# Performance work log

Hardware: AMD Instinct MI355X
Metric: run time of the kernel (lower is better)

The kernel has to match this reference:

```python
import jax, jax.numpy as jnp
import numpy as np

NUM_NODES = 100000
NUM_EDGES = 625000
IN_FEATURES = 128
OUT_FEATURES = 128


def setup_inputs() -> dict:
    key = jax.random.key(0)
    k1, k2, k3, k4 = jax.random.split(key, 4)
    x = jax.random.normal(k1, (NUM_NODES, IN_FEATURES), dtype=jnp.float32)
    edge_index = jax.random.randint(k2, (2, NUM_EDGES), 0, NUM_NODES, dtype=jnp.int64)
    # Xavier uniform for W (fan_in=IN, fan_out=OUT); B initialized to zeros in the
    # original, but we use small random values so gradients flow through both paths.
    limit = float(np.sqrt(6.0 / (IN_FEATURES + OUT_FEATURES)))
    W = jax.random.uniform(k3, (OUT_FEATURES, IN_FEATURES), dtype=jnp.float32,
                           minval=-limit, maxval=limit)
    B = jax.random.uniform(k4, (OUT_FEATURES, IN_FEATURES), dtype=jnp.float32,
                           minval=-limit, maxval=limit)
    return {"x": x, "edge_index": edge_index, "W": W, "B": B}


def reference(x, edge_index, W, B):
    sources, destinations = edge_index[0], edge_index[1]
    # message: gather destination features, scatter-add into source slots
    messages = x[destinations]                                        # [E, F_in]
    agg = jax.ops.segment_sum(messages, sources, num_segments=x.shape[0])  # [N, F_in]
    # in-degree (w.r.t. sources) normalization; zero-degree -> divide by 1
    deg = jax.ops.segment_sum(jnp.ones((sources.shape[0],), dtype=x.dtype),
                              sources, num_segments=x.shape[0])       # [N]
    deg = jnp.where(deg == 0, jnp.ones_like(deg), deg)
    agg = agg / deg[:, None]
    # update: (W @ messages.T + B @ x.T).T == messages @ W.T + x @ B.T
    out = agg @ W.T + x @ B.T                                         # [N, F_out]
    return out
```

## Files before the change

### kernel.cpp

```cpp
#include <hip/hip_runtime.h>

#define F_IN   128
#define F_OUT  128

typedef __attribute__((ext_vector_type(8))) short short8;
typedef __attribute__((ext_vector_type(4))) float floatx4;

__device__ __forceinline__ float bf16u_to_f_lo(unsigned int u) {
    union { unsigned int i; float f; } c; c.i = u << 16; return c.f;
}
__device__ __forceinline__ float bf16u_to_f_hi(unsigned int u) {
    union { unsigned int i; float f; } c; c.i = u & 0xffff0000u; return c.f;
}
__device__ __forceinline__ unsigned short f_to_bf16(float f) {
    union { float f; unsigned int i; } c; c.f = f;
    unsigned int u = c.i;
    u += 0x7fffu + ((u >> 16) & 1u);
    return (unsigned short)(u >> 16);
}
__device__ __forceinline__ unsigned int pack2(unsigned short a, unsigned short b) {
    return (unsigned int)a | ((unsigned int)b << 16);
}

__device__ __forceinline__ void gload_lds16(const void* g, void* l) {
    __builtin_amdgcn_global_load_lds(
        (const __attribute__((address_space(1))) unsigned int*)g,
        (__attribute__((address_space(3))) unsigned int*)l, 16, 0, 0);
}

__global__ void zero_kernel(int* __restrict__ p, long n) {
    long i = (long)blockIdx.x * blockDim.x + threadIdx.x;
    long stride = (long)gridDim.x * blockDim.x;
    for (; i < n; i += stride) p[i] = 0;
}

__global__ void hist_kernel(const int* __restrict__ src, int* __restrict__ cnt, int E) {
    int e = blockIdx.x * blockDim.x + threadIdx.x;
    if (e < E) atomicAdd(&cnt[src[e]], 1);
}

__global__ __launch_bounds__(256) void chunk_sums_kernel(const int* __restrict__ cnt,
                                                         int* __restrict__ partials, int n) {
    __shared__ int s[256];
    int b = blockIdx.x, t = threadIdx.x;
    int base = b * 1024 + t * 4;
    int sum = 0;
#pragma unroll
    for (int j = 0; j < 4; ++j) {
        int i = base + j;
        if (i < n) sum += cnt[i];
    }
    s[t] = sum;
    __syncthreads();
    for (int d = 128; d > 0; d >>= 1) {
        if (t < d) s[t] += s[t + d];
        __syncthreads();
    }
    if (t == 0) partials[b] = s[0];
}

__global__ __launch_bounds__(256) void scan_chunks_kernel(int* __restrict__ off,
                                                          const int* __restrict__ partials,
                                                          int n, int nch) {
    __shared__ int s[256];
    __shared__ int ps[128];
    int b = blockIdx.x, t = threadIdx.x;
    if (t < 128) ps[t] = (t < nch && t < b) ? partials[t] : 0;
    int base = b * 1024 + t * 4;
    int v[4];
#pragma unroll
    for (int j = 0; j < 4; ++j) {
        int i = base + j;
        v[j] = (i < n) ? off[i] : 0;
    }
    int l1 = v[0], l2 = l1 + v[1], l3 = l2 + v[2], tot = l3 + v[3];
    s[t] = tot;
    __syncthreads();
    for (int d = 64; d > 0; d >>= 1) {
        if (t < d) ps[t] += ps[t + d];
        __syncthreads();
    }
    for (int d = 1; d < 256; d <<= 1) {
        int val = s[t];
        int add = (t >= d) ? s[t - d] : 0;
        __syncthreads();
        s[t] = val + add;
        __syncthreads();
    }
    int thr_excl = ((t > 0) ? s[t - 1] : 0) + ps[0];
    if (base + 0 < n) off[base + 0] = thr_excl;
    if (base + 1 < n) off[base + 1] = thr_excl + l1;
    if (base + 2 < n) off[base + 2] = thr_excl + l2;
    if (base + 3 < n) off[base + 3] = thr_excl + l3;
}

__global__ void fill_kernel(const int* __restrict__ ei, int* __restrict__ off,
                            int* __restrict__ dst_sorted, int E) {
    int e = blockIdx.x * blockDim.x + threadIdx.x;
    if (e < E) {
        int s = ei[e];
        int d = ei[E + e];
        int p = atomicAdd(&off[s], 1);
        dst_sorted[p] = d;
    }
}

__global__ __launch_bounds__(256) void convert_x_kernel(const float* __restrict__ x,
                                                        char* __restrict__ outb,
                                                        const float* __restrict__ W,
                                                        const float* __restrict__ Bm,
                                                        uint4* __restrict__ bfrag, int N) {
    if (bfrag && blockIdx.x == gridDim.x - 1) {
        int t = threadIdx.x;
#pragma unroll
        for (int i = 0; i < 16; ++i) {
            int flat = i * 256 + t;
            int lane = flat & 63;
            int idx = flat >> 6;
            int nt = idx >> 3, sfrag = idx & 7;
            int n = nt * 16 + (lane & 15);
            int kbase = sfrag * 32 + (lane >> 4) * 8;
            const float* srcp = (kbase < 128) ? (W + n * 128 + kbase)
                                              : (Bm + n * 128 + (kbase - 128));
            float4 v0 = *(const float4*)srcp;
            float4 v1 = *(const float4*)(srcp + 4);
            uint4 pk;
            pk.x = pack2(f_to_bf16(v0.x), f_to_bf16(v0.y));
            pk.y = pack2(f_to_bf16(v0.z), f_to_bf16(v0.w));
            pk.z = pack2(f_to_bf16(v1.x), f_to_bf16(v1.y));
            pk.w = pack2(f_to_bf16(v1.z), f_to_bf16(v1.w));
            bfrag[flat] = pk;
        }
        return;
    }
    long tid = (long)blockIdx.x * blockDim.x + threadIdx.x;
    if (tid >= (long)N * 32) return;
    int row = (int)(tid >> 5);
    int seg = (int)(tid & 31);
    float4 v = *(const float4*)(x + (size_t)row * 128 + seg * 4);
    unsigned short r[4] = {f_to_bf16(v.x), f_to_bf16(v.y), f_to_bf16(v.z), f_to_bf16(v.w)};
    *(ushort4*)(outb + (size_t)row * 512 + 256 + seg * 8) =
        make_ushort4(r[0], r[1], r[2], r[3]);
}

__global__ __launch_bounds__(256) void gather_bf16_kernel(const int* __restrict__ off,
                                                          const int* __restrict__ dst_sorted,
                                                          char* __restrict__ outb, int N) {
    int node = blockIdx.x * 16 + (threadIdx.x >> 4);
    int lane = threadIdx.x & 15;
    if (node >= N) return;
    int start = (node == 0) ? 0 : off[node - 1];
    int end = off[node];
    float acc[8];
#pragma unroll
    for (int i = 0; i < 8; ++i) acc[i] = 0.0f;

    const char* xb = outb;
    int j = start;
    for (; j + 4 <= end; j += 4) {
        int d0 = dst_sorted[j];
        int d1 = dst_sorted[j + 1];
        int d2 = dst_sorted[j + 2];
        int d3 = dst_sorted[j + 3];
        uint4 a = *(const uint4*)(xb + (size_t)d0 * 512 + 256 + lane * 16);
        uint4 b = *(const uint4*)(xb + (size_t)d1 * 512 + 256 + lane * 16);
        uint4 c = *(const uint4*)(xb + (size_t)d2 * 512 + 256 + lane * 16);
        uint4 d = *(const uint4*)(xb + (size_t)d3 * 512 + 256 + lane * 16);
        acc[0] += bf16u_to_f_lo(a.x); acc[1] += bf16u_to_f_hi(a.x);
        acc[2] += bf16u_to_f_lo(a.y); acc[3] += bf16u_to_f_hi(a.y);
        acc[4] += bf16u_to_f_lo(a.z); acc[5] += bf16u_to_f_hi(a.z);
        acc[6] += bf16u_to_f_lo(a.w); acc[7] += bf16u_to_f_hi(a.w);
        acc[0] += bf16u_to_f_lo(b.x); acc[1] += bf16u_to_f_hi(b.x);
        acc[2] += bf16u_to_f_lo(b.y); acc[3] += bf16u_to_f_hi(b.y);
        acc[4] += bf16u_to_f_lo(b.z); acc[5] += bf16u_to_f_hi(b.z);
        acc[6] += bf16u_to_f_lo(b.w); acc[7] += bf16u_to_f_hi(b.w);
        acc[0] += bf16u_to_f_lo(c.x); acc[1] += bf16u_to_f_hi(c.x);
        acc[2] += bf16u_to_f_lo(c.y); acc[3] += bf16u_to_f_hi(c.y);
        acc[4] += bf16u_to_f_lo(c.z); acc[5] += bf16u_to_f_hi(c.z);
        acc[6] += bf16u_to_f_lo(c.w); acc[7] += bf16u_to_f_hi(c.w);
        acc[0] += bf16u_to_f_lo(d.x); acc[1] += bf16u_to_f_hi(d.x);
        acc[2] += bf16u_to_f_lo(d.y); acc[3] += bf16u_to_f_hi(d.y);
        acc[4] += bf16u_to_f_lo(d.z); acc[5] += bf16u_to_f_hi(d.z);
        acc[6] += bf16u_to_f_lo(d.w); acc[7] += bf16u_to_f_hi(d.w);
    }
    for (; j < end; ++j) {
        int d0 = dst_sorted[j];
        uint4 a = *(const uint4*)(xb + (size_t)d0 * 512 + 256 + lane * 16);
        acc[0] += bf16u_to_f_lo(a.x); acc[1] += bf16u_to_f_hi(a.x);
        acc[2] += bf16u_to_f_lo(a.y); acc[3] += bf16u_to_f_hi(a.y);
        acc[4] += bf16u_to_f_lo(a.z); acc[5] += bf16u_to_f_hi(a.z);
        acc[6] += bf16u_to_f_lo(a.w); acc[7] += bf16u_to_f_hi(a.w);
    }
    int deg = end - start;
    float scale = (deg > 0) ? (1.0f / (float)deg) : 1.0f;
    unsigned short r[8];
#pragma unroll
    for (int i = 0; i < 8; ++i) r[i] = f_to_bf16(acc[i] * scale);
    uint4 pk;
    pk.x = pack2(r[0], r[1]);
    pk.y = pack2(r[2], r[3]);
    pk.z = pack2(r[4], r[5]);
    pk.w = pack2(r[6], r[7]);
    *(uint4*)(outb + (size_t)node * 512 + lane * 16) = pk;
}

__global__ __launch_bounds__(256) void gemm_mfma_kernel(const float* __restrict__ W,
                                                        const float* __restrict__ Bm,
                                                        const uint4* __restrict__ bfrag,
                                                        float* __restrict__ out, int N) {
    __shared__ uint4 Bs[4096];
    int t = threadIdx.x;
    int lane = t & 63;
    int w = t >> 6;
    int m16 = lane & 15;
    int quad = lane >> 4;

    if (bfrag) {
#pragma unroll
        for (int j = 0; j < 16; ++j)
            gload_lds16(bfrag + (w * 16 + j) * 64 + lane, &Bs[(w * 16 + j) * 64]);
    } else {
#pragma unroll
        for (int nt2 = 0; nt2 < 2; ++nt2) {
            int nt = w * 2 + nt2;
            int n = nt * 16 + m16;
#pragma unroll
            for (int s = 0; s < 8; ++s) {
                int kbase = s * 32 + quad * 8;
                const float* srcp = (kbase < 128) ? (W + n * 128 + kbase)
                                                  : (Bm + n * 128 + (kbase - 128));
                float4 v0 = *(const float4*)srcp;
                float4 v1 = *(const float4*)(srcp + 4);
                uint4 pk;
                pk.x = pack2(f_to_bf16(v0.x), f_to_bf16(v0.y));
                pk.y = pack2(f_to_bf16(v0.z), f_to_bf16(v0.w));
                pk.z = pack2(f_to_bf16(v1.x), f_to_bf16(v1.y));
                pk.w = pack2(f_to_bf16(v1.z), f_to_bf16(v1.w));
                Bs[(nt * 8 + s) * 64 + lane] = pk;
            }
        }
    }
    __syncthreads();

    int rowbase = blockIdx.x * 128 + w * 32;
    short8 afrag[2][8];
#pragma unroll
    for (int g = 0; g < 2; ++g) {
        int arow = rowbase + g * 16 + m16;
        if (arow > N - 1) arow = N - 1;
        const char* ab = (const char*)out + (size_t)arow * 512;
#pragma unroll
        for (int s = 0; s < 8; ++s)
            afrag[g][s] = *(const short8*)(ab + s * 64 + quad * 16);
    }

    floatx4 acc[2][8];
#pragma unroll
    for (int g = 0; g < 2; ++g)
#pragma unroll
        for (int nt = 0; nt < 8; ++nt) acc[g][nt] = (floatx4){0.f, 0.f, 0.f, 0.f};

#pragma unroll
    for (int nt = 0; nt < 8; ++nt) {
#pragma unroll
        for (int s = 0; s < 8; ++s) {
            short8 bf = *(const short8*)&Bs[(nt * 8 + s) * 64 + lane];
            acc[0][nt] = __builtin_amdgcn_mfma_f32_16x16x32_bf16(afrag[0][s], bf, acc[0][nt], 0, 0, 0);
            acc[1][nt] = __builtin_amdgcn_mfma_f32_16x16x32_bf16(afrag[1][s], bf, acc[1][nt], 0, 0, 0);
        }
    }

#pragma unroll
    for (int g = 0; g < 2; ++g)
#pragma unroll
        for (int nt = 0; nt < 8; ++nt)
#pragma unroll
            for (int r = 0; r < 4; ++r) {
                int gr = rowbase + g * 16 + quad * 4 + r;
                if (gr < N) out[(size_t)gr * 128 + nt * 16 + m16] = acc[g][nt][r];
            }
}

__global__ void invdeg_kernel(int* __restrict__ deg_io, int N) {
    int i = blockIdx.x * blockDim.x + threadIdx.x;
    if (i < N) {
        int d = deg_io[i];
        float inv = (d > 0) ? (1.0f / (float)d) : 1.0f;
        ((float*)deg_io)[i] = inv;
    }
}

__global__ __launch_bounds__(128) void scatter_atomic_kernel(const float* __restrict__ x,
                                                             const int* __restrict__ ei,
                                                             const float* __restrict__ invdeg,
                                                             float* __restrict__ out, int E) {
    int e = blockIdx.x;
    int f = threadIdx.x;
    int s = ei[e];
    int d = ei[E + e];
    float v = x[(long)d * F_IN + f] * invdeg[s];
    atomicAdd(&out[(long)s * F_IN + f], v);
}

__global__ __launch_bounds__(256) void gemm_fused_kernel(const float* __restrict__ x,
                                                         const float* __restrict__ W,
                                                         const float* __restrict__ Bm,
                                                         float* __restrict__ out, int N) {
    __shared__ float As[64][68];
    __shared__ float Ms[64][132];
    int t = threadIdx.x;
    int row0 = blockIdx.x * 64;
    int c0 = (t & 31) * 4;
    int r0 = (t >> 5) * 8;
    float acc[8][4];
#pragma unroll
    for (int i = 0; i < 8; ++i)
#pragma unroll
        for (int j = 0; j < 4; ++j) acc[i][j] = 0.0f;

    for (int kc = 0; kc < 4; ++kc) {
        const float* Asrc = (kc < 2) ? out : x;
        const float* Msrc = (kc < 2) ? W : Bm;
        int k0 = (kc & 1) * 64;
#pragma unroll
        for (int i = 0; i < 4; ++i) {
            int flat = t + 256 * i;
            int m = flat >> 4, ks = flat & 15;
            int row = row0 + m;
            float4 v = make_float4(0.f, 0.f, 0.f, 0.f);
            if (row < N) v = *(const float4*)&Asrc[(long)row * 128 + k0 + ks * 4];
            As[ks * 4 + 0][m] = v.x;
            As[ks * 4 + 1][m] = v.y;
            As[ks * 4 + 2][m] = v.z;
            As[ks * 4 + 3][m] = v.w;
        }
#pragma unroll
        for (int i = 0; i < 8; ++i) {
            int flat = t + 256 * i;
            int c = flat >> 4, ks = flat & 15;
            float4 v = *(const float4*)&Msrc[(long)c * 128 + k0 + ks * 4];
            Ms[ks * 4 + 0][c] = v.x;
            Ms[ks * 4 + 1][c] = v.y;
            Ms[ks * 4 + 2][c] = v.z;
            Ms[ks * 4 + 3][c] = v.w;
        }
        __syncthreads();
#pragma unroll 8
        for (int kk = 0; kk < 64; ++kk) {
            float4 a0 = *(const float4*)&As[kk][r0];
            float4 a1 = *(const float4*)&As[kk][r0 + 4];
            float4 m0 = *(const float4*)&Ms[kk][c0];
            float a[8] = {a0.x, a0.y, a0.z, a0.w, a1.x, a1.y, a1.z, a1.w};
            float m[4] = {m0.x, m0.y, m0.z, m0.w};
#pragma unroll
            for (int i = 0; i < 8; ++i)
#pragma unroll
                for (int j = 0; j < 4; ++j) acc[i][j] += a[i] * m[j];
        }
        __syncthreads();
    }
#pragma unroll
    for (int i = 0; i < 8; ++i) {
        int row = row0 + r0 + i;
        if (row < N) {
            float4 v = make_float4(acc[i][0], acc[i][1], acc[i][2], acc[i][3]);
            *(float4*)&out[(long)row * 128 + c0] = v;
        }
    }
}


extern "C" void kernel_launch(void* const* d_in, const int* in_sizes, int n_in,
                              void* d_out, int out_size, void* d_ws, size_t ws_size,
                              hipStream_t stream) {
    const float* x = (const float*)d_in[0];
    const int* ei = (const int*)d_in[1];
    const float* W = (const float*)d_in[2];
    const float* Bm = (const float*)d_in[3];
    float* out = (float*)d_out;

    const int N = in_sizes[0] / F_IN;
    const int E = in_sizes[1] / 2;
    const int NCHUNK = (N + 1023) / 1024;

    const size_t need_csr    = ((size_t)N + 128 + (size_t)E) * sizeof(int);
    const size_t need_staged = need_csr + 4096 * sizeof(uint4);
    const size_t need_deg    = (size_t)N * sizeof(int);

    if (ws_size >= need_csr) {
        bool staged = (ws_size >= need_staged);
        uint4* bfrag;
        int* off;
        if (staged) {
            bfrag = (uint4*)d_ws;
            off   = (int*)(bfrag + 4096);
        } else {
            bfrag = nullptr;
            off   = (int*)d_ws;
        }
        int* partials   = off + N;
        int* dst_sorted = partials + 128;

        zero_kernel<<<256, 256, 0, stream>>>(off, N);
        hist_kernel<<<(E + 255) / 256, 256, 0, stream>>>(ei, off, E);
        chunk_sums_kernel<<<NCHUNK, 256, 0, stream>>>(off, partials, N);
        scan_chunks_kernel<<<NCHUNK, 256, 0, stream>>>(off, partials, N, NCHUNK);
        fill_kernel<<<(E + 255) / 256, 256, 0, stream>>>(ei, off, dst_sorted, E);
        {
            long tot = (long)N * 32;
            int nb = (int)((tot + 255) / 256) + (staged ? 1 : 0);
            convert_x_kernel<<<nb, 256, 0, stream>>>(x, (char*)out, W, Bm, bfrag, N);
        }
        gather_bf16_kernel<<<(N + 15) / 16, 256, 0, stream>>>(off, dst_sorted, (char*)out, N);
        gemm_mfma_kernel<<<(N + 127) / 128, 256, 0, stream>>>(W, Bm, bfrag, out, N);
    } else if (ws_size >= need_deg) {
        int* deg = (int*)d_ws;
        zero_kernel<<<256, 256, 0, stream>>>(deg, N);
        hist_kernel<<<(E + 255) / 256, 256, 0, stream>>>(ei, deg, E);
        invdeg_kernel<<<(N + 255) / 256, 256, 0, stream>>>(deg, N);
        zero_kernel<<<512, 256, 0, stream>>>((int*)out, (long)N * F_IN);
        scatter_atomic_kernel<<<E, 128, 0, stream>>>(x, ei, (const float*)deg, out, E);
        gemm_fused_kernel<<<(N + 63) / 64, 256, 0, stream>>>(x, W, Bm, out, N);
    }
}
```

Baseline: 222.3 us.

## Transform before aggregating: compute x·W^T first, then gather-add projected rows

Uses linearity to reorder the work. One fused MFMA GEMM computes x@[W;B]^T: the B part is written to out in fp32, and the W part is stored as a bf16 table yb. A gather kernel then sums yb rows over each node's neighbours, scales by 1/deg and adds the result into out. This removes the separate convert pass and the final GEMM over aggregated features, and folds the weight-fragment staging into the zero kernel. It needs an extra N*256-byte workspace and rounds the projected values to bf16 before aggregation, and the new path only runs when the workspace is large enough.

```diff
diff --git a/kernel.cpp b/kernel.cpp
--- a/kernel.cpp
+++ b/kernel.cpp
@@ -28,7 +28,32 @@
         (__attribute__((address_space(3))) unsigned int*)l, 16, 0, 0);
 }
 
-__global__ void zero_kernel(int* __restrict__ p, long n) {
+__global__ void zero_kernel(int* __restrict__ p, long n,
+                            const float* __restrict__ W,
+                            const float* __restrict__ Bm,
+                            uint4* __restrict__ bfrag) {
+    if (bfrag && blockIdx.x == gridDim.x - 1) {
+        int t = threadIdx.x;
+#pragma unroll
+        for (int i = 0; i < 16; ++i) {
+            int flat = i * 256 + t;
+            int lane = flat & 63;
+            int idx = flat >> 6;
+            int nt = idx >> 2, s = idx & 3;
+            int n2 = nt * 16 + (lane & 15);
+            int kbase = s * 32 + (lane >> 4) * 8;
+            const float* srcp = (n2 < 128) ? (W + (size_t)n2 * 128 + kbase)
+                                           : (Bm + (size_t)(n2 - 128) * 128 + kbase);
+            float4 v0 = *(const float4*)srcp;
+            float4 v1 = *(const float4*)(srcp + 4);
+            uint4 pk;
+            pk.x = pack2(f_to_bf16(v0.x), f_to_bf16(v0.y));
+            pk.y = pack2(f_to_bf16(v0.z), f_to_bf16(v0.w));
+            pk.z = pack2(f_to_bf16(v1.x), f_to_bf16(v1.y));
+            pk.w = pack2(f_to_bf16(v1.z), f_to_bf16(v1.w));
+            bfrag[flat] = pk;
+        }
+    }
     long i = (long)blockIdx.x * blockDim.x + threadIdx.x;
     long stride = (long)gridDim.x * blockDim.x;
     for (; i < n; i += stride) p[i] = 0;
@@ -103,6 +128,148 @@
         int p = atomicAdd(&off[s], 1);
         dst_sorted[p] = d;
     }
+}
+
+__global__ __launch_bounds__(256, 2) void gemm_xwb_kernel(const float* __restrict__ x,
+                                                          const uint4* __restrict__ bfrag,
+                                                          char* __restrict__ yb,
+                                                          float* __restrict__ out, int N) {
+    __shared__ uint4 Bs[4096];
+    int t = threadIdx.x;
+    int lane = t & 63;
+    int w = t >> 6;
+    int m16 = lane & 15;
+    int quad = lane >> 4;
+
+#pragma unroll
+    for (int j = 0; j < 16; ++j)
+        gload_lds16(bfrag + (w * 16 + j) * 64 + lane, &Bs[(w * 16 + j) * 64]);
+
+    int rowbase = blockIdx.x * 128 + w * 32;
+    short8 afrag[2][4];
+#pragma unroll
+    for (int g = 0; g < 2; ++g) {
+        int arow = rowbase + g * 16 + m16;
+        if (arow > N - 1) arow = N - 1;
+        const float* xr = x + (size_t)arow * 128;
+#pragma unroll
+        for (int s = 0; s < 4; ++s) {
+            float4 v0 = *(const float4*)(xr + s * 32 + quad * 8);
+            float4 v1 = *(const float4*)(xr + s * 32 + quad * 8 + 4);
+            short8 f;
+            f[0] = (short)f_to_bf16(v0.x); f[1] = (short)f_to_bf16(v0.y);
+            f[2] = (short)f_to_bf16(v0.z); f[3] = (short)f_to_bf16(v0.w);
+            f[4] = (short)f_to_bf16(v1.x); f[5] = (short)f_to_bf16(v1.y);
+            f[6] = (short)f_to_bf16(v1.z); f[7] = (short)f_to_bf16(v1.w);
+            afrag[g][s] = f;
+        }
+    }
+    __syncthreads();
+
+    floatx4 acc[2][16];
+#pragma unroll
+    for (int g = 0; g < 2; ++g)
+#pragma unroll
+        for (int nt = 0; nt < 16; ++nt) acc[g][nt] = (floatx4){0.f, 0.f, 0.f, 0.f};
+
+#pragma unroll
+    for (int nt = 0; nt < 16; ++nt) {
+#pragma unroll
+        for (int s = 0; s < 4; ++s) {
+            short8 bf = *(const short8*)&Bs[(nt * 4 + s) * 64 + lane];
+            acc[0][nt] = __builtin_amdgcn_mfma_f32_16x16x32_bf16(afrag[0][s], bf, acc[0][nt], 0, 0, 0);
+            acc[1][nt] = __builtin_amdgcn_mfma_f32_16x16x32_bf16(afrag[1][s], bf, acc[1][nt], 0, 0, 0);
+        }
+    }
+
+#pragma unroll
+    for (int g = 0; g < 2; ++g)
+#pragma unroll
+        for (int nt = 8; nt < 16; ++nt)
+#pragma unroll
+            for (int r = 0; r < 4; ++r) {
+                int gr = rowbase + g * 16 + quad * 4 + r;
+                if (gr < N) out[(size_t)gr * 128 + (nt - 8) * 16 + m16] = acc[g][nt][r];
+            }
+
+    __syncthreads();
+    unsigned short* lu = (unsigned short*)Bs + w * 4096;
+#pragma unroll
+    for (int g = 0; g < 2; ++g)
+#pragma unroll
+        for (int nt = 0; nt < 8; ++nt)
+#pragma unroll
+            for (int r = 0; r < 4; ++r)
+                lu[(g * 16 + quad * 4 + r) * 128 + nt * 16 + m16] = f_to_bf16(acc[g][nt][r]);
+    __syncthreads();
+#pragma unroll
+    for (int p = 0; p < 8; ++p) {
+        int lrow = p * 4 + quad;
+        uint4 v = *(const uint4*)(lu + lrow * 128 + m16 * 8);
+        int grow = rowbase + lrow;
+        if (grow < N) *(uint4*)(yb + (size_t)grow * 256 + m16 * 16) = v;
+    }
+}
+
+__global__ __launch_bounds__(256) void gather_add_kernel(const int* __restrict__ off,
+                                                         const int* __restrict__ dst_sorted,
+                                                         const char* __restrict__ yb,
+                                                         float* __restrict__ out, int N) {
+    int node = blockIdx.x * 16 + (threadIdx.x >> 4);
+    int lane = threadIdx.x & 15;
+    if (node >= N) return;
+    int start = (node == 0) ? 0 : off[node - 1];
+    int end = off[node];
+    float acc[8];
+#pragma unroll
+    for (int i = 0; i < 8; ++i) acc[i] = 0.0f;
+
+    int j = start;
+    for (; j + 4 <= end; j += 4) {
+        int d0 = dst_sorted[j];
+        int d1 = dst_sorted[j + 1];
+        int d2 = dst_sorted[j + 2];
+        int d3 = dst_sorted[j + 3];
+        uint4 a = *(const uint4*)(yb + (size_t)d0 * 256 + lane * 16);
+        uint4 b = *(const uint4*)(yb + (size_t)d1 * 256 + lane * 16);
+        uint4 c = *(const uint4*)(yb + (size_t)d2 * 256 + lane * 16);
+        uint4 d = *(const uint4*)(yb + (size_t)d3 * 256 + lane * 16);
+        acc[0] += bf16u_to_f_lo(a.x); acc[1] += bf16u_to_f_hi(a.x);
+        acc[2] += bf16u_to_f_lo(a.y); acc[3] += bf16u_to_f_hi(a.y);
+        acc[4] += bf16u_to_f_lo(a.z); acc[5] += bf16u_to_f_hi(a.z);
+        acc[6] += bf16u_to_f_lo(a.w); acc[7] += bf16u_to_f_hi(a.w);
+        acc[0] += bf16u_to_f_lo(b.x); acc[1] += bf16u_to_f_hi(b.x);
+        acc[2] += bf16u_to_f_lo(b.y); acc[3] += bf16u_to_f_hi(b.y);
+        acc[4] += bf16u_to_f_lo(b.z); acc[5] += bf16u_to_f_hi(b.z);
+        acc[6] += bf16u_to_f_lo(b.w); acc[7] += bf16u_to_f_hi(b.w);
+        acc[0] += bf16u_to_f_lo(c.x); acc[1] += bf16u_to_f_hi(c.x);
+        acc[2] += bf16u_to_f_lo(c.y); acc[3] += bf16u_to_f_hi(c.y);
+        acc[4] += bf16u_to_f_lo(c.z); acc[5] += bf16u_to_f_hi(c.z);
+        acc[6] += bf16u_to_f_lo(c.w); acc[7] += bf16u_to_f_hi(c.w);
+        acc[0] += bf16u_to_f_lo(d.x); acc[1] += bf16u_to_f_hi(d.x);
+        acc[2] += bf16u_to_f_lo(d.y); acc[3] += bf16u_to_f_hi(d.y);
+        acc[4] += bf16u_to_f_lo(d.z); acc[5] += bf16u_to_f_hi(d.z);
+        acc[6] += bf16u_to_f_lo(d.w); acc[7] += bf16u_to_f_hi(d.w);
+    }
+    for (; j < end; ++j) {
+        int d0 = dst_sorted[j];
+        uint4 a = *(const uint4*)(yb + (size_t)d0 * 256 + lane * 16);
+        acc[0] += bf16u_to_f_lo(a.x); acc[1] += bf16u_to_f_hi(a.x);
+        acc[2] += bf16u_to_f_lo(a.y); acc[3] += bf16u_to_f_hi(a.y);
+        acc[4] += bf16u_to_f_lo(a.z); acc[5] += bf16u_to_f_hi(a.z);
+        acc[6] += bf16u_to_f_lo(a.w); acc[7] += bf16u_to_f_hi(a.w);
+    }
+    int deg = end - start;
+    float scale = (deg > 0) ? (1.0f / (float)deg) : 1.0f;
+    float* orow = out + (size_t)node * 128 + lane * 8;
+    float4 z0 = *(const float4*)orow;
+    float4 z1 = *(const float4*)(orow + 4);
+    float4 r0 = make_float4(acc[0] * scale + z0.x, acc[1] * scale + z0.y,
+                            acc[2] * scale + z0.z, acc[3] * scale + z0.w);
+    float4 r1 = make_float4(acc[4] * scale + z1.x, acc[5] * scale + z1.y,
+                            acc[6] * scale + z1.z, acc[7] * scale + z1.w);
+    *(float4*)orow = r0;
+    *(float4*)(orow + 4) = r1;
 }
 
 __global__ __launch_bounds__(256) void convert_x_kernel(const float* __restrict__ x,
@@ -154,7 +321,6 @@
     float acc[8];
 #pragma unroll
     for (int i = 0; i < 8; ++i) acc[i] = 0.0f;
-
     const char* xb = outb;
     int j = start;
     for (; j + 4 <= end; j += 4) {
@@ -385,9 +551,24 @@
 
     const size_t need_csr    = ((size_t)N + 128 + (size_t)E) * sizeof(int);
     const size_t need_staged = need_csr + 4096 * sizeof(uint4);
+    const size_t need_big    = need_staged + (size_t)N * 256;
     const size_t need_deg    = (size_t)N * sizeof(int);
 
-    if (ws_size >= need_csr) {
+    if (ws_size >= need_big) {
+        uint4* bfrag    = (uint4*)d_ws;
+        char*  yb       = (char*)(bfrag + 4096);
+        int*   off      = (int*)(yb + (size_t)N * 256);
+        int*   partials = off + N;
+        int*   dst_sorted = partials + 128;
+
+        zero_kernel<<<256, 256, 0, stream>>>(off, N, W, Bm, bfrag);
+        hist_kernel<<<(E + 255) / 256, 256, 0, stream>>>(ei, off, E);
+        chunk_sums_kernel<<<NCHUNK, 256, 0, stream>>>(off, partials, N);
+        scan_chunks_kernel<<<NCHUNK, 256, 0, stream>>>(off, partials, N, NCHUNK);
+        fill_kernel<<<(E + 255) / 256, 256, 0, stream>>>(ei, off, dst_sorted, E);
+        gemm_xwb_kernel<<<(N + 127) / 128, 256, 0, stream>>>(x, bfrag, yb, out, N);
+        gather_add_kernel<<<(N + 15) / 16, 256, 0, stream>>>(off, dst_sorted, yb, out, N);
+    } else if (ws_size >= need_csr) {
         bool staged = (ws_size >= need_staged);
         uint4* bfrag;
         int* off;
@@ -401,7 +582,7 @@
         int* partials   = off + N;
         int* dst_sorted = partials + 128;
 
-        zero_kernel<<<256, 256, 0, stream>>>(off, N);
+        zero_kernel<<<256, 256, 0, stream>>>(off, N, nullptr, nullptr, nullptr);
         hist_kernel<<<(E + 255) / 256, 256, 0, stream>>>(ei, off, E);
         chunk_sums_kernel<<<NCHUNK, 256, 0, stream>>>(off, partials, N);
         scan_chunks_kernel<<<NCHUNK, 256, 0, stream>>>(off, partials, N, NCHUNK);
@@ -415,10 +596,10 @@
         gemm_mfma_kernel<<<(N + 127) / 128, 256, 0, stream>>>(W, Bm, bfrag, out, N);
     } else if (ws_size >= need_deg) {
         int* deg = (int*)d_ws;
-        zero_kernel<<<256, 256, 0, stream>>>(deg, N);
+        zero_kernel<<<256, 256, 0, stream>>>(deg, N, nullptr, nullptr, nullptr);
         hist_kernel<<<(E + 255) / 256, 256, 0, stream>>>(ei, deg, E);
         invdeg_kernel<<<(N + 255) / 256, 256, 0, stream>>>(deg, N);
-        zero_kernel<<<512, 256, 0, stream>>>((int*)out, (long)N * F_IN);
+        zero_kernel<<<512, 256, 0, stream>>>((int*)out, (long)N * F_IN, nullptr, nullptr, nullptr);
         scatter_atomic_kernel<<<E, 128, 0, stream>>>(x, ei, (const float*)deg, out, E);
         gemm_fused_kernel<<<(N + 63) / 64, 256, 0, stream>>>(x, W, Bm, out, N);
     }
```

After: 229.8 us. 3.4% more time.

## Fuse init and scan kernels, persistent GEMM tiles, two nodes per gather group

Applied to the files above, without the earlier changes.

Zeroing the count array is merged into the x-to-bf16 conversion kernel, and the two-pass chunk-sum/scan is replaced by one scan kernel in which each block recomputes its prefix from earlier chunks. The gather kernel processes two nodes per 16-lane group, and the GEMM becomes a grid-strided kernel that loads the B fragments into LDS once per block and reuses them for two row tiles. This is meant to cut launch overhead and repeated B staging. The cost is redundant prefix reads in the scan and less parallelism in the gather and GEMM grids. The path that runs without staged weights is dropped.

```diff
diff --git a/kernel.cpp b/kernel.cpp
--- a/kernel.cpp
+++ b/kernel.cpp
@@ -28,89 +28,14 @@
         (__attribute__((address_space(3))) unsigned int*)l, 16, 0, 0);
 }
 
-__global__ void zero_kernel(int* __restrict__ p, long n) {
-    long i = (long)blockIdx.x * blockDim.x + threadIdx.x;
-    long stride = (long)gridDim.x * blockDim.x;
-    for (; i < n; i += stride) p[i] = 0;
-}
-
-__global__ void hist_kernel(const int* __restrict__ src, int* __restrict__ cnt, int E) {
-    int e = blockIdx.x * blockDim.x + threadIdx.x;
-    if (e < E) atomicAdd(&cnt[src[e]], 1);
-}
-
-__global__ __launch_bounds__(256) void chunk_sums_kernel(const int* __restrict__ cnt,
-                                                         int* __restrict__ partials, int n) {
-    __shared__ int s[256];
-    int b = blockIdx.x, t = threadIdx.x;
-    int base = b * 1024 + t * 4;
-    int sum = 0;
-#pragma unroll
-    for (int j = 0; j < 4; ++j) {
-        int i = base + j;
-        if (i < n) sum += cnt[i];
-    }
-    s[t] = sum;
-    __syncthreads();
-    for (int d = 128; d > 0; d >>= 1) {
-        if (t < d) s[t] += s[t + d];
-        __syncthreads();
-    }
-    if (t == 0) partials[b] = s[0];
-}
-
-__global__ __launch_bounds__(256) void scan_chunks_kernel(int* __restrict__ off,
-                                                          const int* __restrict__ partials,
-                                                          int n, int nch) {
-    __shared__ int s[256];
-    __shared__ int ps[128];
-    int b = blockIdx.x, t = threadIdx.x;
-    if (t < 128) ps[t] = (t < nch && t < b) ? partials[t] : 0;
-    int base = b * 1024 + t * 4;
-    int v[4];
-#pragma unroll
-    for (int j = 0; j < 4; ++j) {
-        int i = base + j;
-        v[j] = (i < n) ? off[i] : 0;
-    }
-    int l1 = v[0], l2 = l1 + v[1], l3 = l2 + v[2], tot = l3 + v[3];
-    s[t] = tot;
-    __syncthreads();
-    for (int d = 64; d > 0; d >>= 1) {
-        if (t < d) ps[t] += ps[t + d];
-        __syncthreads();
-    }
-    for (int d = 1; d < 256; d <<= 1) {
-        int val = s[t];
-        int add = (t >= d) ? s[t - d] : 0;
-        __syncthreads();
-        s[t] = val + add;
-        __syncthreads();
-    }
-    int thr_excl = ((t > 0) ? s[t - 1] : 0) + ps[0];
-    if (base + 0 < n) off[base + 0] = thr_excl;
-    if (base + 1 < n) off[base + 1] = thr_excl + l1;
-    if (base + 2 < n) off[base + 2] = thr_excl + l2;
-    if (base + 3 < n) off[base + 3] = thr_excl + l3;
-}
-
-__global__ void fill_kernel(const int* __restrict__ ei, int* __restrict__ off,
-                            int* __restrict__ dst_sorted, int E) {
-    int e = blockIdx.x * blockDim.x + threadIdx.x;
-    if (e < E) {
-        int s = ei[e];
-        int d = ei[E + e];
-        int p = atomicAdd(&off[s], 1);
-        dst_sorted[p] = d;
-    }
-}
-
-__global__ __launch_bounds__(256) void convert_x_kernel(const float* __restrict__ x,
-                                                        char* __restrict__ outb,
-                                                        const float* __restrict__ W,
-                                                        const float* __restrict__ Bm,
-                                                        uint4* __restrict__ bfrag, int N) {
-    if (bfrag && blockIdx.x == gridDim.x - 1) {
+__global__ __launch_bounds__(256) void init_kernel(const float* __restrict__ x,
+                                                   char* __restrict__ outb,
+                                                   const float* __restrict__ W,
+                                                   const float* __restrict__ Bm,
+                                                   uint4* __restrict__ bfrag,
+                                                   int* __restrict__ cnt, int N) {
+    long tid = (long)blockIdx.x * blockDim.x + threadIdx.x;
+    if (blockIdx.x == gridDim.x - 1) {
         int t = threadIdx.x;
 #pragma unroll
         for (int i = 0; i < 16; ++i) {
@@ -133,81 +58,143 @@
         }
         return;
     }
-    long tid = (long)blockIdx.x * blockDim.x + threadIdx.x;
-    if (tid >= (long)N * 32) return;
-    int row = (int)(tid >> 5);
-    int seg = (int)(tid & 31);
-    float4 v = *(const float4*)(x + (size_t)row * 128 + seg * 4);
-    unsigned short r[4] = {f_to_bf16(v.x), f_to_bf16(v.y), f_to_bf16(v.z), f_to_bf16(v.w)};
-    *(ushort4*)(outb + (size_t)row * 512 + 256 + seg * 8) =
-        make_ushort4(r[0], r[1], r[2], r[3]);
+    if (tid < N) cnt[tid] = 0;
+    if (tid < (long)N * 32) {
+        int row = (int)(tid >> 5);
+        int seg = (int)(tid & 31);
+        float4 v = *(const float4*)(x + (size_t)row * 128 + seg * 4);
+        unsigned short r[4] = {f_to_bf16(v.x), f_to_bf16(v.y), f_to_bf16(v.z), f_to_bf16(v.w)};
+        *(ushort4*)(outb + (size_t)row * 512 + 256 + seg * 8) =
+            make_ushort4(r[0], r[1], r[2], r[3]);
+    }
+}
+
+__global__ void hist_kernel(const int* __restrict__ src, int* __restrict__ cnt, int E) {
+    int e = blockIdx.x * blockDim.x + threadIdx.x;
+    if (e < E) atomicAdd(&cnt[src[e]], 1);
+}
+
+__global__ __launch_bounds__(256) void scan_kernel(const int* __restrict__ cnt,
+                                                   int* __restrict__ off, int n) {
+    __shared__ int s[256];
+    __shared__ int red[256];
+    int b = blockIdx.x, t = threadIdx.x;
+    long pre = (long)b * 1024;
+    int sum = 0;
+    for (long i = (long)t * 4; i < pre; i += 1024) {
+        int4 v = *(const int4*)&cnt[i];
+        sum += v.x + v.y + v.z + v.w;
+    }
+    red[t] = sum;
+    __syncthreads();
+    for (int d = 128; d > 0; d >>= 1) {
+        if (t < d) red[t] += red[t + d];
+        __syncthreads();
+    }
+    int base = red[0];
+    int cbase = b * 1024 + t * 4;
+    int v[4];
+#pragma unroll
+    for (int j = 0; j < 4; ++j) {
+        int i = cbase + j;
+        v[j] = (i < n) ? cnt[i] : 0;
+    }
+    int l1 = v[0], l2 = l1 + v[1], l3 = l2 + v[2], tot = l3 + v[3];
+    s[t] = tot;
+    __syncthreads();
+    for (int d = 1; d < 256; d <<= 1) {
+        int val = s[t];
+        int add = (t >= d) ? s[t - d] : 0;
+        __syncthreads();
+        s[t] = val + add;
+        __syncthreads();
+    }
+    int thr_excl = ((t > 0) ? s[t - 1] : 0) + base;
+    if (cbase + 0 < n) off[cbase + 0] = thr_excl;
+    if (cbase + 1 < n) off[cbase + 1] = thr_excl + l1;
+    if (cbase + 2 < n) off[cbase + 2] = thr_excl + l2;
+    if (cbase + 3 < n) off[cbase + 3] = thr_excl + l3;
+}
+
+__global__ void fill_kernel(const int* __restrict__ ei, int* __restrict__ off,
+                            int* __restrict__ dst_sorted, int E) {
+    int e = blockIdx.x * blockDim.x + threadIdx.x;
+    if (e < E) {
+        int s = ei[e];
+        int d = ei[E + e];
+        int p = atomicAdd(&off[s], 1);
+        dst_sorted[p] = d;
+    }
 }
 
 __global__ __launch_bounds__(256) void gather_bf16_kernel(const int* __restrict__ off,
                                                           const int* __restrict__ dst_sorted,
                                                           char* __restrict__ outb, int N) {
-    int node = blockIdx.x * 16 + (threadIdx.x >> 4);
+    int gid = blockIdx.x * 16 + (threadIdx.x >> 4);
     int lane = threadIdx.x & 15;
-    if (node >= N) return;
-    int start = (node == 0) ? 0 : off[node - 1];
-    int end = off[node];
-    float acc[8];
-#pragma unroll
-    for (int i = 0; i < 8; ++i) acc[i] = 0.0f;
-
-    const char* xb = outb;
-    int j = start;
-    for (; j + 4 <= end; j += 4) {
-        int d0 = dst_sorted[j];
-        int d1 = dst_sorted[j + 1];
-        int d2 = dst_sorted[j + 2];
-        int d3 = dst_sorted[j + 3];
-        uint4 a = *(const uint4*)(xb + (size_t)d0 * 512 + 256 + lane * 16);
-        uint4 b = *(const uint4*)(xb + (size_t)d1 * 512 + 256 + lane * 16);
-        uint4 c = *(const uint4*)(xb + (size_t)d2 * 512 + 256 + lane * 16);
-        uint4 d = *(const uint4*)(xb + (size_t)d3 * 512 + 256 + lane * 16);
-        acc[0] += bf16u_to_f_lo(a.x); acc[1] += bf16u_to_f_hi(a.x);
-        acc[2] += bf16u_to_f_lo(a.y); acc[3] += bf16u_to_f_hi(a.y);
-        acc[4] += bf16u_to_f_lo(a.z); acc[5] += bf16u_to_f_hi(a.z);
-        acc[6] += bf16u_to_f_lo(a.w); acc[7] += bf16u_to_f_hi(a.w);
-        acc[0] += bf16u_to_f_lo(b.x); acc[1] += bf16u_to_f_hi(b.x);
-        acc[2] += bf16u_to_f_lo(b.y); acc[3] += bf16u_to_f_hi(b.y);
-        acc[4] += bf16u_to_f_lo(b.z); acc[5] += bf16u_to_f_hi(b.z);
-        acc[6] += bf16u_to_f_lo(b.w); acc[7] += bf16u_to_f_hi(b.w);
-        acc[0] += bf16u_to_f_lo(c.x); acc[1] += bf16u_to_f_hi(c.x);
-        acc[2] += bf16u_to_f_lo(c.y); acc[3] += bf16u_to_f_hi(c.y);
-        acc[4] += bf16u_to_f_lo(c.z); acc[5] += bf16u_to_f_hi(c.z);
-        acc[6] += bf16u_to_f_lo(c.w); acc[7] += bf16u_to_f_hi(c.w);
-        acc[0] += bf16u_to_f_lo(d.x); acc[1] += bf16u_to_f_hi(d.x);
-        acc[2] += bf16u_to_f_lo(d.y); acc[3] += bf16u_to_f_hi(d.y);
-        acc[4] += bf16u_to_f_lo(d.z); acc[5] += bf16u_to_f_hi(d.z);
-        acc[6] += bf16u_to_f_lo(d.w); acc[7] += bf16u_to_f_hi(d.w);
-    }
-    for (; j < end; ++j) {
-        int d0 = dst_sorted[j];
-        uint4 a = *(const uint4*)(xb + (size_t)d0 * 512 + 256 + lane * 16);
-        acc[0] += bf16u_to_f_lo(a.x); acc[1] += bf16u_to_f_hi(a.x);
-        acc[2] += bf16u_to_f_lo(a.y); acc[3] += bf16u_to_f_hi(a.y);
-        acc[4] += bf16u_to_f_lo(a.z); acc[5] += bf16u_to_f_hi(a.z);
-        acc[6] += bf16u_to_f_lo(a.w); acc[7] += bf16u_to_f_hi(a.w);
-    }
-    int deg = end - start;
-    float scale = (deg > 0) ? (1.0f / (float)deg) : 1.0f;
-    unsigned short r[8];
-#pragma unroll
-    for (int i = 0; i < 8; ++i) r[i] = f_to_bf16(acc[i] * scale);
-    uint4 pk;
-    pk.x = pack2(r[0], r[1]);
-    pk.y = pack2(r[2], r[3]);
-    pk.z = pack2(r[4], r[5]);
-    pk.w = pack2(r[6], r[7]);
-    *(uint4*)(outb + (size_t)node * 512 + lane * 16) = pk;
-}
-
-__global__ __launch_bounds__(256) void gemm_mfma_kernel(const float* __restrict__ W,
-                                                        const float* __restrict__ Bm,
-                                                        const uint4* __restrict__ bfrag,
-                                                        float* __restrict__ out, int N) {
+#pragma unroll
+    for (int which = 0; which < 2; ++which) {
+        int node = gid * 2 + which;
+        if (node >= N) return;
+        int start = (node == 0) ? 0 : off[node - 1];
+        int end = off[node];
+        float acc[8];
+#pragma unroll
+        for (int i = 0; i < 8; ++i) acc[i] = 0.0f;
+
+        const char* xb = outb;
+        int j = start;
+        for (; j + 4 <= end; j += 4) {
+            int d0 = dst_sorted[j];
+            int d1 = dst_sorted[j + 1];
+            int d2 = dst_sorted[j + 2];
+            int d3 = dst_sorted[j + 3];
+            uint4 a = *(const uint4*)(xb + (size_t)d0 * 512 + 256 + lane * 16);
+            uint4 b = *(const uint4*)(xb + (size_t)d1 * 512 + 256 + lane * 16);
+            uint4 c = *(const uint4*)(xb + (size_t)d2 * 512 + 256 + lane * 16);
+            uint4 d = *(const uint4*)(xb + (size_t)d3 * 512 + 256 + lane * 16);
+            acc[0] += bf16u_to_f_lo(a.x); acc[1] += bf16u_to_f_hi(a.x);
+            acc[2] += bf16u_to_f_lo(a.y); acc[3] += bf16u_to_f_hi(a.y);
+            acc[4] += bf16u_to_f_lo(a.z); acc[5] += bf16u_to_f_hi(a.z);
+            acc[6] += bf16u_to_f_lo(a.w); acc[7] += bf16u_to_f_hi(a.w);
+            acc[0] += bf16u_to_f_lo(b.x); acc[1] += bf16u_to_f_hi(b.x);
+            acc[2] += bf16u_to_f_lo(b.y); acc[3] += bf16u_to_f_hi(b.y);
+            acc[4] += bf16u_to_f_lo(b.z); acc[5] += bf16u_to_f_hi(b.z);
+            acc[6] += bf16u_to_f_lo(b.w); acc[7] += bf16u_to_f_hi(b.w);
+            acc[0] += bf16u_to_f_lo(c.x); acc[1] += bf16u_to_f_hi(c.x);
+            acc[2] += bf16u_to_f_lo(c.y); acc[3] += bf16u_to_f_hi(c.y);
+            acc[4] += bf16u_to_f_lo(c.z); acc[5] += bf16u_to_f_hi(c.z);
+            acc[6] += bf16u_to_f_lo(c.w); acc[7] += bf16u_to_f_hi(c.w);
+            acc[0] += bf16u_to_f_lo(d.x); acc[1] += bf16u_to_f_hi(d.x);
+            acc[2] += bf16u_to_f_lo(d.y); acc[3] += bf16u_to_f_hi(d.y);
+            acc[4] += bf16u_to_f_lo(d.z); acc[5] += bf16u_to_f_hi(d.z);
+            acc[6] += bf16u_to_f_lo(d.w); acc[7] += bf16u_to_f_hi(d.w);
+        }
+        for (; j < end; ++j) {
+            int d0 = dst_sorted[j];
+            uint4 a = *(const uint4*)(xb + (size_t)d0 * 512 + 256 + lane * 16);
+            acc[0] += bf16u_to_f_lo(a.x); acc[1] += bf16u_to_f_hi(a.x);
+            acc[2] += bf16u_to_f_lo(a.y); acc[3] += bf16u_to_f_hi(a.y);
+            acc[4] += bf16u_to_f_lo(a.z); acc[5] += bf16u_to_f_hi(a.z);
+            acc[6] += bf16u_to_f_lo(a.w); acc[7] += bf16u_to_f_hi(a.w);
+        }
+        int deg = end - start;
+        float scale = (deg > 0) ? (1.0f / (float)deg) : 1.0f;
+        unsigned short r[8];
+#pragma unroll
+        for (int i = 0; i < 8; ++i) r[i] = f_to_bf16(acc[i] * scale);
+        uint4 pk;
+        pk.x = pack2(r[0], r[1]);
+        pk.y = pack2(r[2], r[3]);
+        pk.z = pack2(r[4], r[5]);
+        pk.w = pack2(r[6], r[7]);
+        *(uint4*)(outb + (size_t)node * 512 + lane * 16) = pk;
+    }
+}
+
+__global__ __launch_bounds__(256, 2) void gemm_tiles_kernel(const uint4* __restrict__ bfrag,
+                                                            float* __restrict__ out,
+                                                            int N, int ntiles) {
     __shared__ uint4 Bs[4096];
     int t = threadIdx.x;
     int lane = t & 63;
@@ -215,70 +202,56 @@
     int m16 = lane & 15;
     int quad = lane >> 4;
 
-    if (bfrag) {
-#pragma unroll
-        for (int j = 0; j < 16; ++j)
-            gload_lds16(bfrag + (w * 16 + j) * 64 + lane, &Bs[(w * 16 + j) * 64]);
-    } else {
-#pragma unroll
-        for (int nt2 = 0; nt2 < 2; ++nt2) {
-            int nt = w * 2 + nt2;
-            int n = nt * 16 + m16;
+#pragma unroll
+    for (int j = 0; j < 16; ++j)
+        gload_lds16(bfrag + (w * 16 + j) * 64 + lane, &Bs[(w * 16 + j) * 64]);
+    __syncthreads();
+
+    for (int ti = blockIdx.x; ti < ntiles; ti += gridDim.x) {
+        int rowbase = ti * 128 + w * 32;
+        short8 afrag[2][8];
+#pragma unroll
+        for (int g = 0; g < 2; ++g) {
+            int arow = rowbase + g * 16 + m16;
+            if (arow > N - 1) arow = N - 1;
+            const char* ab = (const char*)out + (size_t)arow * 512;
+#pragma unroll
+            for (int s = 0; s < 8; ++s)
+                afrag[g][s] = *(const short8*)(ab + s * 64 + quad * 16);
+        }
+
+        floatx4 acc[2][8];
+#pragma unroll
+        for (int g = 0; g < 2; ++g)
+#pragma unroll
+            for (int nt = 0; nt < 8; ++nt) acc[g][nt] = (floatx4){0.f, 0.f, 0.f, 0.f};
+
+#pragma unroll
+        for (int nt = 0; nt < 8; ++nt) {
 #pragma unroll
             for (int s = 0; s < 8; ++s) {
-                int kbase = s * 32 + quad * 8;
-                const float* srcp = (kbase < 128) ? (W + n * 128 + kbase)
-                                                  : (Bm + n * 128 + (kbase - 128));
-                float4 v0 = *(const float4*)srcp;
-                float4 v1 = *(const float4*)(srcp + 4);
-                uint4 pk;
-                pk.x = pack2(f_to_bf16(v0.x), f_to_bf16(v0.y));
-                pk.y = pack2(f_to_bf16(v0.z), f_to_bf16(v0.w));
-                pk.z = pack2(f_to_bf16(v1.x), f_to_bf16(v1.y));
-                pk.w = pack2(f_to_bf16(v1.z), f_to_bf16(v1.w));
-                Bs[(nt * 8 + s) * 64 + lane] = pk;
+                short8 bf = *(const short8*)&Bs[(nt * 8 + s) * 64 + lane];
+                acc[0][nt] = __builtin_amdgcn_mfma_f32_16x16x32_bf16(afrag[0][s], bf, acc[0][nt], 0, 0, 0);
+                acc[1][nt] = __builtin_amdgcn_mfma_f32_16x16x32_bf16(afrag[1][s], bf, acc[1][nt], 0, 0, 0);
             }
         }
-    }
-    __syncthreads();
-
-    int rowbase = blockIdx.x * 128 + w * 32;
-    short8 afrag[2][8];
-#pragma unroll
-    for (int g = 0; g < 2; ++g) {
-        int arow = rowbase + g * 16 + m16;
-        if (arow > N - 1) arow = N - 1;
-        const char* ab = (const char*)out + (size_t)arow * 512;
-#pragma unroll
-        for (int s = 0; s < 8; ++s)
-            afrag[g][s] = *(const short8*)(ab + s * 64 + quad * 16);
-    }
-
-    floatx4 acc[2][8];
-#pragma unroll
-    for (int g = 0; g < 2; ++g)
-#pragma unroll
-        for (int nt = 0; nt < 8; ++nt) acc[g][nt] = (floatx4){0.f, 0.f, 0.f, 0.f};
-
-#pragma unroll
-    for (int nt = 0; nt < 8; ++nt) {
-#pragma unroll
-        for (int s = 0; s < 8; ++s) {
-            short8 bf = *(const short8*)&Bs[(nt * 8 + s) * 64 + lane];
-            acc[0][nt] = __builtin_amdgcn_mfma_f32_16x16x32_bf16(afrag[0][s], bf, acc[0][nt], 0, 0, 0);
-            acc[1][nt] = __builtin_amdgcn_mfma_f32_16x16x32_bf16(afrag[1][s], bf, acc[1][nt], 0, 0, 0);
-        }
-    }
-
-#pragma unroll
-    for (int g = 0; g < 2; ++g)
-#pragma unroll
-        for (int nt = 0; nt < 8; ++nt)
-#pragma unroll
-            for (int r = 0; r < 4; ++r) {
-                int gr = rowbase + g * 16 + quad * 4 + r;
-                if (gr < N) out[(size_t)gr * 128 + nt * 16 + m16] = acc[g][nt][r];
-            }
+
+#pragma unroll
+        for (int g = 0; g < 2; ++g)
+#pragma unroll
+            for (int nt = 0; nt < 8; ++nt)
+#pragma unroll
+                for (int r = 0; r < 4; ++r) {
+                    int gr = rowbase + g * 16 + quad * 4 + r;
+                    if (gr < N) out[(size_t)gr * 128 + nt * 16 + m16] = acc[g][nt][r];
+                }
+    }
+}
+
+__global__ void zero_kernel(int* __restrict__ p, long n) {
+    long i = (long)blockIdx.x * blockDim.x + threadIdx.x;
+    long stride = (long)gridDim.x * blockDim.x;
+    for (; i < n; i += stride) p[i] = 0;
 }
 
 __global__ void invdeg_kernel(int* __restrict__ deg_io, int N) {
@@ -383,36 +356,30 @@
     const int E = in_sizes[1] / 2;
     const int NCHUNK = (N + 1023) / 1024;
 
-    const size_t need_csr    = ((size_t)N + 128 + (size_t)E) * sizeof(int);
-    const size_t need_staged = need_csr + 4096 * sizeof(uint4);
-    const size_t need_deg    = (size_t)N * sizeof(int);
-
-    if (ws_size >= need_csr) {
-        bool staged = (ws_size >= need_staged);
-        uint4* bfrag;
-        int* off;
-        if (staged) {
-            bfrag = (uint4*)d_ws;
-            off   = (int*)(bfrag + 4096);
-        } else {
-            bfrag = nullptr;
-            off   = (int*)d_ws;
-        }
-        int* partials   = off + N;
-        int* dst_sorted = partials + 128;
-
-        zero_kernel<<<256, 256, 0, stream>>>(off, N);
-        hist_kernel<<<(E + 255) / 256, 256, 0, stream>>>(ei, off, E);
-        chunk_sums_kernel<<<NCHUNK, 256, 0, stream>>>(off, partials, N);
-        scan_chunks_kernel<<<NCHUNK, 256, 0, stream>>>(off, partials, N, NCHUNK);
-        fill_kernel<<<(E + 255) / 256, 256, 0, stream>>>(ei, off, dst_sorted, E);
+    const size_t need_main = 4096 * sizeof(uint4) + ((size_t)2 * N + (size_t)E) * sizeof(int);
+    const size_t need_deg  = (size_t)N * sizeof(int);
+
+    if (ws_size >= need_main) {
+        uint4* bfrag      = (uint4*)d_ws;
+        int*   cnt        = (int*)(bfrag + 4096);
+        int*   off        = cnt + N;
+        int*   dst_sorted = off + N;
+
         {
             long tot = (long)N * 32;
-            int nb = (int)((tot + 255) / 256) + (staged ? 1 : 0);
-            convert_x_kernel<<<nb, 256, 0, stream>>>(x, (char*)out, W, Bm, bfrag, N);
-        }
-        gather_bf16_kernel<<<(N + 15) / 16, 256, 0, stream>>>(off, dst_sorted, (char*)out, N);
-        gemm_mfma_kernel<<<(N + 127) / 128, 256, 0, stream>>>(W, Bm, bfrag, out, N);
+            int nb = (int)((tot + 255) / 256) + 1;
+            init_kernel<<<nb, 256, 0, stream>>>(x, (char*)out, W, Bm, bfrag, cnt, N);
+        }
+        hist_kernel<<<(E + 255) / 256, 256, 0, stream>>>(ei, cnt, E);
+        scan_kernel<<<NCHUNK, 256, 0, stream>>>(cnt, off, N);
+        fill_kernel<<<(E + 255) / 256, 256, 0, stream>>>(ei, off, dst_sorted, E);
+        gather_bf16_kernel<<<(N + 31) / 32, 256, 0, stream>>>(off, dst_sorted, (char*)out, N);
+        {
+            int ntiles = (N + 127) / 128;
+            int grid = (ntiles + 1) / 2;
+            if (grid < 1) grid = 1;
+            gemm_tiles_kernel<<<grid, 256, 0, stream>>>(bfrag, out, N, ntiles);
+        }
     } else if (ws_size >= need_deg) {
         int* deg = (int*)d_ws;
         zero_kernel<<<256, 256, 0, stream>>>(deg, N);
```

Result: slower. 261.0 us (+17.4%).
